# Optimization experiments

Hardware: AMD Instinct MI355X
Metric: run time of the kernel (lower is better)

Reference implementation:

```python
import jax, jax.numpy as jnp
import numpy as np

B, D_IN, D_OUT = 8192, 512, 1024
N_PATHS, N_STEPS = 256, 50  # n_paths = min(output_size, 256); n_steps fixed at 50
T_HORIZON, DECAY_RATE = 1.0, 0.1


def setup_inputs() -> dict:
    key = jax.random.key(0)
    k_x, k_wfb, k_wagg, k_noise = jax.random.split(key, 4)
    x = jax.random.normal(k_x, (B, D_IN), dtype=jnp.float32)
    W_fb = jax.random.normal(k_wfb, (1, D_IN), dtype=jnp.float32) / np.sqrt(D_IN)
    b_fb = jnp.zeros((1,), dtype=jnp.float32)
    W_agg = jax.random.normal(k_wagg, (D_OUT, N_PATHS), dtype=jnp.float32) / np.sqrt(N_PATHS)
    b_agg = jnp.zeros((D_OUT,), dtype=jnp.float32)
    # Pre-drawn standard normal increments for all batch items / paths / steps
    noise = jax.random.normal(k_noise, (B, N_PATHS, N_STEPS), dtype=jnp.float32)
    return {"x": x, "W_fb": W_fb, "b_fb": b_fb, "W_agg": W_agg, "b_agg": b_agg, "noise": noise}


def reference(x, W_fb, b_fb, W_agg, b_agg, noise):
    # feedback_transform + sigmoid -> scalar feedback per sample  [B]
    feedback = jax.nn.sigmoid(x @ W_fb.T + b_fb)[:, 0]
    # original extracts feedback via .item(): no grad flows into the simulation
    fb = jax.lax.stop_gradient(feedback)

    dt = jnp.asarray(T_HORIZON / N_STEPS, dtype=x.dtype)
    t = jnp.arange(N_STEPS, dtype=x.dtype) * dt                 # [S]
    # per-sample, per-step drift-free diffusion scale: 0.5 + fb * exp(-decay * t)
    scale = 0.5 + fb[:, None] * jnp.exp(-DECAY_RATE * t)[None, :]  # [B, S]

    # endpoint of X_{t+1} = X_t + sqrt(dt) * scale_t * noise_t, X_0 = 0
    # == sqrt(dt) * sum_t scale[b,t] * noise[b,p,t]
    endpoints = jnp.einsum('bps,bs->bp', noise, scale) * jnp.sqrt(dt)  # [B, P]

    # path_aggregator linear
    return endpoints @ W_agg.T + b_agg  # [B, D_OUT]
```

## Files before the change

### kernel.cpp

```cpp
#include <hip/hip_runtime.h>
#include <math.h>


#define B_TOTAL 8192
#define D_IN    512
#define D_OUT   1024
#define NP      256
#define NS      50
#define BT      16
#define THREADS 256
#define PCHUNK  8
#define NCHUNK  (NP / PCHUNK)
#define CHUNK_F4 1600
#define CHUNK_F4P 1792
#define ROW_F4   100
#define EP_STRIDE 264

#define SQRT_DT 0.14142135623730951f

typedef __bf16 bf16x8 __attribute__((ext_vector_type(8)));
typedef float  f32x4  __attribute__((ext_vector_type(4)));

__device__ __forceinline__ unsigned short f2bf(float f) {
    unsigned u = __float_as_uint(f);
    return (unsigned short)((u + 0x7FFFu + ((u >> 16) & 1u)) >> 16);
}

__device__ __forceinline__ void async_cp16(const float4* g, float* l) {
    __builtin_amdgcn_global_load_lds(
        (const __attribute__((address_space(1))) void*)g,
        (__attribute__((address_space(3))) void*)l,
        16, 0, 0);
}

__global__ __launch_bounds__(THREADS, 2) void bicep_main(
    const float* __restrict__ x,
    const float* __restrict__ Wfb,
    const float* __restrict__ bfb,
    const float* __restrict__ Wagg,
    const float* __restrict__ bagg,
    const float* __restrict__ noise,
    float* __restrict__ out)
{
    __shared__ __align__(16) float nbuf[2][CHUNK_F4P * 4];
    __shared__ __align__(16) unsigned short ep_bf[BT * EP_STRIDE];
    __shared__ float fb_s[BT];
    __shared__ float bagg_s[D_OUT];

    const int tid  = threadIdx.x;
    const int lane = tid & 63;
    const int wave = tid >> 6;
    const int b0   = blockIdx.x * BT;

    {
        #pragma unroll
        for (int i = 0; i < D_OUT / THREADS; ++i)
            bagg_s[i * THREADS + tid] = bagg[i * THREADS + tid];

        const float bf_b = bfb[0];
        const float4* wf = (const float4*)Wfb + lane * 2;
        float4 wa = wf[0], wb = wf[1];
        #pragma unroll
        for (int rr = 0; rr < 4; ++rr) {
            int row = wave * 4 + rr;
            const float4* xr = (const float4*)(x + (size_t)(b0 + row) * D_IN) + lane * 2;
            float4 xa = xr[0], xb = xr[1];
            float p = xa.x*wa.x + xa.y*wa.y + xa.z*wa.z + xa.w*wa.w
                    + xb.x*wb.x + xb.y*wb.y + xb.z*wb.z + xb.w*wb.w;
            #pragma unroll
            for (int mm = 32; mm >= 1; mm >>= 1) p += __shfl_xor(p, mm, 64);
            if (lane == 0) fb_s[row] = 1.0f / (1.0f + __expf(-(p + bf_b)));
        }
    }

    const int h     = tid & 1;
    const int jpair = tid >> 1;
    const int c_row = jpair >> 3;
    const int c_pl  = jpair & 7;

    float ereg[25];
    #pragma unroll
    for (int s = 0; s < 25; ++s)
        ereg[s] = __expf(-0.002f * (float)(h * 25 + s));

    const float4* nptr[7];
    #pragma unroll
    for (int r = 0; r < 7; ++r) {
        int g4  = r * 256 + tid;
        int row = g4 / 100;
        int off = g4 - row * 100;
        if (row > BT - 1) { row = BT - 1; off = 0; }
        nptr[r] = (const float4*)(noise + (size_t)(b0 + row) * (NP * NS)) + off;
    }

    __syncthreads();

    #pragma unroll
    for (int r = 0; r < 7; ++r)
        async_cp16(nptr[r], nbuf[0] + (r * 256 + wave * 64) * 4);

    for (int c = 0; c < NCHUNK; ++c) {
        const float* nb = nbuf[c & 1];

        if (c + 1 < NCHUNK) {
            float* nbn = nbuf[(c + 1) & 1];
            #pragma unroll
            for (int r = 0; r < 7; ++r)
                async_cp16(nptr[r] + (c + 1) * ROW_F4, nbn + (r * 256 + wave * 64) * 4);
            asm volatile("s_waitcnt vmcnt(7)" ::: "memory");
        } else {
            asm volatile("s_waitcnt vmcnt(0)" ::: "memory");
        }
        __builtin_amdgcn_s_barrier();
        asm volatile("" ::: "memory");

        const float* src = &nb[c_row * (PCHUNK * NS) + c_pl * NS + h * 25];
        float s0 = 0.f, s1 = 0.f;
        #pragma unroll
        for (int s = 0; s < 25; ++s) {
            float nv = src[s];
            s0 += nv;
            s1 = fmaf(ereg[s], nv, s1);
        }
        s0 += __shfl_xor(s0, 1, 64);
        s1 += __shfl_xor(s1, 1, 64);
        if (h == 0) {
            float ep = SQRT_DT * fmaf(fb_s[c_row], s1, 0.5f * s0);
            ep_bf[c_row * EP_STRIDE + c * PCHUNK + c_pl] = f2bf(ep);
        }

        asm volatile("" ::: "memory");
        __builtin_amdgcn_s_barrier();
    }
    __syncthreads();

    {
        const int m  = lane & 15;
        const int kg = lane >> 4;

        bf16x8 afr[8];
        #pragma unroll
        for (int ks = 0; ks < 8; ++ks)
            afr[ks] = *(const bf16x8*)&ep_bf[m * EP_STRIDE + ks * 32 + kg * 8];

        #pragma unroll 2
        for (int i = 0; i < 16; ++i) {
            int O = wave * 16 + i;
            const float* wp = Wagg + (size_t)(O * 16 + m) * NP + kg * 8;
            f32x4 acc = {0.f, 0.f, 0.f, 0.f};
            #pragma unroll
            for (int ks = 0; ks < 8; ++ks) {
                float4 wa = *(const float4*)(wp + ks * 32);
                float4 wb = *(const float4*)(wp + ks * 32 + 4);
                bf16x8 bfr = { (__bf16)wa.x, (__bf16)wa.y, (__bf16)wa.z, (__bf16)wa.w,
                               (__bf16)wb.x, (__bf16)wb.y, (__bf16)wb.z, (__bf16)wb.w };
                acc = __builtin_amdgcn_mfma_f32_16x16x32_bf16(afr[ks], bfr, acc, 0, 0, 0);
            }
            float bias = bagg_s[O * 16 + m];
            #pragma unroll
            for (int r = 0; r < 4; ++r)
                out[(size_t)(b0 + kg * 4 + r) * D_OUT + O * 16 + m] = acc[r] + bias;
        }
    }
}

extern "C" void kernel_launch(void* const* d_in, const int* in_sizes, int n_in,
                              void* d_out, int out_size, void* d_ws, size_t ws_size,
                              hipStream_t stream) {
    const float* x     = (const float*)d_in[0];
    const float* Wfb   = (const float*)d_in[1];
    const float* bfb   = (const float*)d_in[2];
    const float* Wagg  = (const float*)d_in[3];
    const float* bagg  = (const float*)d_in[4];
    const float* noise = (const float*)d_in[5];
    float* out = (float*)d_out;
    (void)d_ws; (void)ws_size;

    bicep_main<<<dim3(B_TOTAL / BT), dim3(THREADS), 0, stream>>>(
        x, Wfb, bfb, Wagg, bagg, noise, out);
}
```

Before: 618.7 us.

## Interleave aggregator MFMA into noise streaming loop with persistent accumulators

Instead of running the full Wagg GEMM after all noise chunks have been reduced, each wave now issues one 32-wide k-slice of MFMAs every four chunks, as soon as those endpoint columns exist. The 16 output-tile accumulators stay in registers across the loop, and the bias add and stores happen once at the end. The goal is to hide the GEMM and its Wagg loads behind the noise streaming. The cost is 64 extra accumulator registers. The Wagg global loads inside the loop may also force the compiler to wait for all outstanding loads, which would drain the async noise prefetch on those iterations.

```diff
diff --git a/kernel.cpp b/kernel.cpp
--- a/kernel.cpp
+++ b/kernel.cpp
@@ -83,6 +83,12 @@
     for (int s = 0; s < 25; ++s)
         ereg[s] = __expf(-0.002f * (float)(h * 25 + s));
 
+    const int m  = lane & 15;
+    const int kg = lane >> 4;
+    f32x4 acc[16];
+    #pragma unroll
+    for (int i = 0; i < 16; ++i) acc[i] = (f32x4){0.f, 0.f, 0.f, 0.f};
+
     const float4* nptr[7];
     #pragma unroll
     for (int r = 0; r < 7; ++r) {
@@ -129,38 +135,33 @@
             ep_bf[c_row * EP_STRIDE + c * PCHUNK + c_pl] = f2bf(ep);
         }
 
+        asm volatile("s_waitcnt lgkmcnt(0)" ::: "memory");
+        __builtin_amdgcn_s_barrier();
         asm volatile("" ::: "memory");
-        __builtin_amdgcn_s_barrier();
-    }
-    __syncthreads();
 
-    {
-        const int m  = lane & 15;
-        const int kg = lane >> 4;
-
-        bf16x8 afr[8];
-        #pragma unroll
-        for (int ks = 0; ks < 8; ++ks)
-            afr[ks] = *(const bf16x8*)&ep_bf[m * EP_STRIDE + ks * 32 + kg * 8];
-
-        #pragma unroll 2
-        for (int i = 0; i < 16; ++i) {
-            int O = wave * 16 + i;
-            const float* wp = Wagg + (size_t)(O * 16 + m) * NP + kg * 8;
-            f32x4 acc = {0.f, 0.f, 0.f, 0.f};
+        if ((c & 3) == 3) {
+            const int g = c >> 2;
+            bf16x8 afr = *(const bf16x8*)&ep_bf[m * EP_STRIDE + g * 32 + kg * 8];
+            const float* wbase = Wagg + (size_t)(wave * 256 + m) * NP + g * 32 + kg * 8;
             #pragma unroll
-            for (int ks = 0; ks < 8; ++ks) {
-                float4 wa = *(const float4*)(wp + ks * 32);
-                float4 wb = *(const float4*)(wp + ks * 32 + 4);
+            for (int i = 0; i < 16; ++i) {
+                const float* wp = wbase + (size_t)i * 16 * NP;
+                float4 wa = *(const float4*)(wp);
+                float4 wb = *(const float4*)(wp + 4);
                 bf16x8 bfr = { (__bf16)wa.x, (__bf16)wa.y, (__bf16)wa.z, (__bf16)wa.w,
                                (__bf16)wb.x, (__bf16)wb.y, (__bf16)wb.z, (__bf16)wb.w };
-                acc = __builtin_amdgcn_mfma_f32_16x16x32_bf16(afr[ks], bfr, acc, 0, 0, 0);
+                acc[i] = __builtin_amdgcn_mfma_f32_16x16x32_bf16(afr, bfr, acc[i], 0, 0, 0);
             }
-            float bias = bagg_s[O * 16 + m];
-            #pragma unroll
-            for (int r = 0; r < 4; ++r)
-                out[(size_t)(b0 + kg * 4 + r) * D_OUT + O * 16 + m] = acc[r] + bias;
         }
+    }
+
+    #pragma unroll
+    for (int i = 0; i < 16; ++i) {
+        const int O = wave * 16 + i;
+        const float bias = bagg_s[O * 16 + m];
+        #pragma unroll
+        for (int r = 0; r < 4; ++r)
+            out[(size_t)(b0 + kg * 4 + r) * D_OUT + O * 16 + m] = acc[i][r] + bias;
     }
 }
 
```

Measured after the change: 592.7 us. -4.2%, faster.
